# Kernel optimization log

Measured on AMD Instinct MI355X. Metric: run time of the kernel, lower is better.

Reference implementation:

```python
import jax, jax.numpy as jnp
import numpy as np

E, N, NB = 250000, 20000, 8
D_EDGE, D_RBF, D_CBF, D_TRI = 128, 16, 16, 64
INV_SQRT_2 = 1.0 / np.sqrt(2.0).astype(np.float32)
INV_SQRT_NB = 1.0 / np.sqrt(float(NB))


def setup_inputs() -> dict:
    key = jax.random.key(0)
    ks = jax.random.split(key, 13)
    def w(k, fi, fo):
        return (jax.random.normal(k, (fi, fo), dtype=jnp.float32) / np.sqrt(fi)).astype(jnp.float32)
    return {
        "m_st": jax.random.normal(ks[0], (E, D_EDGE), dtype=jnp.float32),
        "rbf": jax.random.normal(ks[1], (E, D_RBF), dtype=jnp.float32),
        "cbf": jax.random.normal(ks[2], (E, NB, D_CBF), dtype=jnp.float32),
        "idx_s": jax.random.randint(ks[3], (E,), 0, N),
        "idx_swap": jax.random.randint(ks[4], (E,), 0, E),
        "basis_idx1": jax.random.randint(ks[5], (N, NB), 0, E),
        "W_m_rbf": w(ks[6], D_EDGE, D_EDGE),
        "W_rbf": w(ks[7], D_RBF, D_EDGE),
        "W_m_cbf": w(ks[8], D_EDGE, D_TRI),
        "W_cbf": w(ks[9], D_CBF, D_TRI),
        "W_dir": w(ks[10], D_TRI, D_EDGE),
        "W_st": w(ks[11], D_EDGE, D_EDGE),
        "W_ts": w(ks[12], D_EDGE, D_EDGE),
    }


def reference(m_st, rbf, cbf, idx_s, idx_swap, basis_idx1,
              W_m_rbf, W_rbf, W_m_cbf, W_cbf, W_dir, W_st, W_ts):
    act = jax.nn.silu
    # gather per-edge basis indices: (E, NB) -> (E*NB,)
    b1 = basis_idx1[idx_s].reshape(-1)
    # rbf branch (ScaleFactor == 1.0 at init -> identity)
    m = act(m_st @ W_m_rbf)                     # (E, D_EDGE)
    m = m * (rbf @ W_rbf)                       # (E, D_EDGE)
    # cbf branch
    e, nb, c = cbf.shape
    cbf2 = cbf.reshape(e * nb, c)               # (E*NB, D_CBF)
    m_nb = act(m @ W_m_cbf)                     # (E, D_TRI)
    m_nb = m_nb[b1]                             # gather -> (E*NB, D_TRI)
    m_nb = m_nb * (cbf2 @ W_cbf)                # (E*NB, D_TRI)
    x = m_nb.reshape(e, nb, -1).sum(1) * INV_SQRT_NB  # (E, D_TRI)
    x = act(x @ W_dir)                          # (E, D_EDGE)
    x_st = act(x @ W_st)
    x_ts = act(x @ W_ts)[idx_swap]              # swap-gather
    return (x_st + x_ts) * INV_SQRT_2
```

## Files before the change

### kernel.cpp

```cpp
#include <hip/hip_runtime.h>


#define DEV __device__ __forceinline__

typedef __attribute__((ext_vector_type(8))) short bf16x8;
typedef __attribute__((ext_vector_type(4))) float f32x4;

constexpr int E = 250000;
constexpr float INV_SQRT_2  = 0.70710678118654752f;
constexpr float INV_SQRT_NB = 0.35355339059327373f;

constexpr int PW1 = 0;
constexpr int PW2 = 16384;
constexpr int PW3 = 20480;
constexpr int PWD = 28672;
constexpr int PWS = 36864;
constexpr int PWT = 53248;
constexpr int PWC = 69632;
constexpr int PACK_TOTAL = 72192;

constexpr size_t OFF_T = 1u << 18;

DEV unsigned short f2bf(float f) {
  unsigned u = __float_as_uint(f);
  return (unsigned short)((u + 0x7fffu + ((u >> 16) & 1u)) >> 16);
}
DEV float bf2f(unsigned short h) { return __uint_as_float((unsigned)h << 16); }
DEV float silu_f(float x) { return x / (1.f + __expf(-x)); }

__global__ __launch_bounds__(256) void k0_pack(
    const float* __restrict__ W1, const float* __restrict__ W2,
    const float* __restrict__ W3, const float* __restrict__ Wc,
    const float* __restrict__ Wd, const float* __restrict__ Ws,
    const float* __restrict__ Wt, unsigned short* __restrict__ pack) {
  int idx = blockIdx.x * 256 + threadIdx.x;
  if (idx >= PACK_TOTAL) return;
  float v = 0.f;
  if (idx < PW2)      { int i = idx;       int n = i >> 7, k = i & 127; v = W1[k * 128 + n]; }
  else if (idx < PW3) { int i = idx - PW2; int n = i >> 5, k = i & 31;  v = (k < 16) ? W2[k * 128 + n] : 0.f; }
  else if (idx < PWD) { int i = idx - PW3; int n = i >> 7, k = i & 127; v = W3[k * 64 + n]; }
  else if (idx < PWS) { int i = idx - PWD; int n = i >> 6, k = i & 63;  v = Wd[k * 128 + n]; }
  else if (idx < PWT) { int i = idx - PWS; int n = i >> 7, k = i & 127; v = Ws[k * 128 + n]; }
  else if (idx < PWC) { int i = idx - PWT; int n = i >> 7, k = i & 127; v = Wt[k * 128 + n]; }
  else                { int i = idx - PWC; int n = i / 40, k = i % 40;  v = (k < 16) ? Wc[k * 64 + n] : 0.f; }
  pack[idx] = f2bf(v);
}

__global__ __launch_bounds__(512) void k1_mbranch(
    const float* __restrict__ m_st, const float* __restrict__ rbf,
    const unsigned short* __restrict__ pack, unsigned short* __restrict__ tT) {
  __shared__ __align__(16) unsigned short sA[128 * 136];
  __shared__ __align__(16) unsigned short sR[128 * 40];
  const int tid = threadIdx.x;
  const int e0 = blockIdx.x * 128;

  #pragma unroll
  for (int it = 0; it < 16; ++it) {
    int i = tid + it * 512;
    int row = i >> 6, kh = i & 63;
    int er = min(e0 + row, E - 1);
    const float2 v = *(const float2*)(m_st + (size_t)er * 128 + kh * 2);
    unsigned pk = (unsigned)f2bf(v.x) | ((unsigned)f2bf(v.y) << 16);
    *(unsigned*)(sA + row * 136 + kh * 2) = pk;
  }
  #pragma unroll
  for (int it = 0; it < 4; ++it) {
    int i = tid + it * 512;
    int row = i >> 4, kh = i & 15;
    int er = min(e0 + row, E - 1);
    unsigned pk = 0;
    if (kh < 8) {
      const float2 v = *(const float2*)(rbf + (size_t)er * 16 + kh * 2);
      pk = (unsigned)f2bf(v.x) | ((unsigned)f2bf(v.y) << 16);
    }
    *(unsigned*)(sR + row * 40 + kh * 2) = pk;
  }
  __syncthreads();

  const int lane = tid & 63, wv = tid >> 6;
  const int m = lane & 15, q = lane >> 4;
  const int arow = wv * 16 + m;

  const f32x4 zero4 = {0.f, 0.f, 0.f, 0.f};
  f32x4 macc[8], racc[8];
  #pragma unroll
  for (int nt = 0; nt < 8; ++nt) { macc[nt] = zero4; racc[nt] = zero4; }

  {
    bf16x8 a = *(const bf16x8*)(sR + arow * 40 + q * 8);
    #pragma unroll
    for (int nt = 0; nt < 8; ++nt) {
      bf16x8 b = *(const bf16x8*)(pack + PW2 + (nt * 16 + m) * 32 + q * 8);
      racc[nt] = __builtin_amdgcn_mfma_f32_16x16x32_bf16(a, b, racc[nt], 0, 0, 0);
    }
  }
  #pragma unroll
  for (int kk = 0; kk < 4; ++kk) {
    bf16x8 a = *(const bf16x8*)(sA + arow * 136 + kk * 32 + q * 8);
    #pragma unroll
    for (int nt = 0; nt < 8; ++nt) {
      bf16x8 b = *(const bf16x8*)(pack + PW1 + (nt * 16 + m) * 128 + kk * 32 + q * 8);
      macc[nt] = __builtin_amdgcn_mfma_f32_16x16x32_bf16(a, b, macc[nt], 0, 0, 0);
    }
  }
  #pragma unroll
  for (int nt = 0; nt < 8; ++nt)
    #pragma unroll
    for (int r = 0; r < 4; ++r) {
      float v = silu_f(macc[nt][r]) * racc[nt][r];
      sA[(wv * 16 + q * 4 + r) * 136 + nt * 16 + m] = f2bf(v);
    }
  __syncthreads();

  f32x4 tacc[4];
  #pragma unroll
  for (int nt = 0; nt < 4; ++nt) tacc[nt] = zero4;
  #pragma unroll
  for (int kk = 0; kk < 4; ++kk) {
    bf16x8 a = *(const bf16x8*)(sA + arow * 136 + kk * 32 + q * 8);
    #pragma unroll
    for (int nt = 0; nt < 4; ++nt) {
      bf16x8 b = *(const bf16x8*)(pack + PW3 + (nt * 16 + m) * 128 + kk * 32 + q * 8);
      tacc[nt] = __builtin_amdgcn_mfma_f32_16x16x32_bf16(a, b, tacc[nt], 0, 0, 0);
    }
  }
  #pragma unroll
  for (int r = 0; r < 4; ++r) {
    int erow = e0 + wv * 16 + q * 4 + r;
    if (erow < E) {
      ushort4 o;
      o.x = f2bf(silu_f(tacc[0][r]));
      o.y = f2bf(silu_f(tacc[1][r]));
      o.z = f2bf(silu_f(tacc[2][r]));
      o.w = f2bf(silu_f(tacc[3][r]));
      *(ushort4*)(tT + (size_t)erow * 64 + m * 4) = o;
    }
  }
}

DEV void xtile_gather_reduce(
    const float* __restrict__ cbf, const int* __restrict__ sB,
    const unsigned short* __restrict__ tT, const bf16x8* bw,
    unsigned short* __restrict__ sX,
    int wv, int m, int q, long long rowA, long long rowB, int mt) {
  bf16x8 af = {0, 0, 0, 0, 0, 0, 0, 0};
  if (q < 2) {
    long long row = (m < 8) ? rowA + m : rowB + (m - 8);
    const float4 c0 = *(const float4*)(cbf + row * 16 + q * 8);
    const float4 c1 = *(const float4*)(cbf + row * 16 + q * 8 + 4);
    af[0] = (short)f2bf(c0.x); af[1] = (short)f2bf(c0.y);
    af[2] = (short)f2bf(c0.z); af[3] = (short)f2bf(c0.w);
    af[4] = (short)f2bf(c1.x); af[5] = (short)f2bf(c1.y);
    af[6] = (short)f2bf(c1.z); af[7] = (short)f2bf(c1.w);
  }
  const f32x4 zero4 = {0.f, 0.f, 0.f, 0.f};
  f32x4 p0 = zero4, p1 = zero4, p2 = zero4, p3 = zero4;
  p0 = __builtin_amdgcn_mfma_f32_16x16x32_bf16(af, bw[0], p0, 0, 0, 0);
  p1 = __builtin_amdgcn_mfma_f32_16x16x32_bf16(af, bw[1], p1, 0, 0, 0);
  p2 = __builtin_amdgcn_mfma_f32_16x16x32_bf16(af, bw[2], p2, 0, 0, 0);
  p3 = __builtin_amdgcn_mfma_f32_16x16x32_bf16(af, bw[3], p3, 0, 0, 0);

  float s0 = 0.f, s1 = 0.f, s2 = 0.f, s3 = 0.f;
  const int lrb = wv * 128 + mt * 16;
  #pragma unroll
  for (int r = 0; r < 4; ++r) {
    int brow = sB[lrb + q * 4 + r];
    ushort4 tv = *(const ushort4*)(tT + (size_t)brow * 64 + m * 4);
    s0 += bf2f(tv.x) * p0[r];
    s1 += bf2f(tv.y) * p1[r];
    s2 += bf2f(tv.z) * p2[r];
    s3 += bf2f(tv.w) * p3[r];
  }
  s0 += __shfl_xor(s0, 16);
  s1 += __shfl_xor(s1, 16);
  s2 += __shfl_xor(s2, 16);
  s3 += __shfl_xor(s3, 16);

  int lrow = wv * 16 + mt * 2 + (q >> 1);
  if (q == 0 || q == 2) {
    sX[lrow * 72 +  0 + m] = f2bf(s0 * INV_SQRT_NB);
    sX[lrow * 72 + 16 + m] = f2bf(s1 * INV_SQRT_NB);
    sX[lrow * 72 + 32 + m] = f2bf(s2 * INV_SQRT_NB);
    sX[lrow * 72 + 48 + m] = f2bf(s3 * INV_SQRT_NB);
  }
}

DEV void ytile(const unsigned short* __restrict__ pack,
               const unsigned short* __restrict__ sX,
               unsigned short* __restrict__ sY, int wv, int m, int q) {
  const int arow = wv * 16 + m;
  const f32x4 zero4 = {0.f, 0.f, 0.f, 0.f};
  f32x4 yacc[8];
  #pragma unroll
  for (int nt = 0; nt < 8; ++nt) yacc[nt] = zero4;
  #pragma unroll
  for (int kk = 0; kk < 2; ++kk) {
    bf16x8 a = *(const bf16x8*)(sX + arow * 72 + kk * 32 + q * 8);
    #pragma unroll
    for (int nt = 0; nt < 8; ++nt) {
      bf16x8 b = *(const bf16x8*)(pack + PWD + (nt * 16 + m) * 64 + kk * 32 + q * 8);
      yacc[nt] = __builtin_amdgcn_mfma_f32_16x16x32_bf16(a, b, yacc[nt], 0, 0, 0);
    }
  }
  #pragma unroll
  for (int nt = 0; nt < 8; ++nt)
    #pragma unroll
    for (int r = 0; r < 4; ++r)
      sY[(wv * 16 + q * 4 + r) * 136 + nt * 16 + m] = f2bf(silu_f(yacc[nt][r]));
}

__global__ __launch_bounds__(512) void k2_fused(
    const float* __restrict__ cbf, const int* __restrict__ idx_s,
    const int* __restrict__ basis_idx1, const unsigned short* __restrict__ pack,
    const unsigned short* __restrict__ tT, float* __restrict__ out) {
  __shared__ __align__(16) unsigned short sWc[64 * 40];
  __shared__ int sB1[1024];
  __shared__ __align__(16) unsigned short sX[128 * 72];
  __shared__ __align__(16) unsigned short sY[128 * 136];
  const int tid = threadIdx.x;
  const int e0 = blockIdx.x * 128;

  ((uint2*)sWc)[tid] = ((const uint2*)(pack + PWC))[tid];
  if (tid < 128) ((uint2*)sWc)[512 + tid] = ((const uint2*)(pack + PWC))[512 + tid];
  #pragma unroll
  for (int it = 0; it < 2; ++it) {
    int i = tid + it * 512;
    int e = min(e0 + (i >> 3), E - 1);
    int b = basis_idx1[idx_s[e] * 8 + (i & 7)];
    sB1[i] = min(max(b, 0), E - 1);
  }
  __syncthreads();

  const int lane = tid & 63, wv = tid >> 6;
  const int m = lane & 15, q = lane >> 4;

  bf16x8 bw[4];
  #pragma unroll
  for (int nt = 0; nt < 4; ++nt)
    bw[nt] = *(const bf16x8*)(sWc + (nt * 16 + m) * 40 + q * 8);

  for (int mt = 0; mt < 8; ++mt) {
    int ea = min(e0 + wv * 16 + mt * 2, E - 1);
    int eb = min(ea + 1, E - 1);
    xtile_gather_reduce(cbf, sB1, tT, bw, sX, wv, m, q,
                        (long long)ea * 8, (long long)eb * 8, mt);
  }
  __syncthreads();

  ytile(pack, sX, sY, wv, m, q);
  __syncthreads();

  const int arow = wv * 16 + m;
  const f32x4 zero4 = {0.f, 0.f, 0.f, 0.f};
  f32x4 acc[8];
  #pragma unroll
  for (int nt = 0; nt < 8; ++nt) acc[nt] = zero4;
  #pragma unroll
  for (int kk = 0; kk < 4; ++kk) {
    bf16x8 a = *(const bf16x8*)(sY + arow * 136 + kk * 32 + q * 8);
    #pragma unroll
    for (int nt = 0; nt < 8; ++nt) {
      bf16x8 b = *(const bf16x8*)(pack + PWS + (nt * 16 + m) * 128 + kk * 32 + q * 8);
      acc[nt] = __builtin_amdgcn_mfma_f32_16x16x32_bf16(a, b, acc[nt], 0, 0, 0);
    }
  }
  #pragma unroll
  for (int nt = 0; nt < 8; ++nt)
    #pragma unroll
    for (int r = 0; r < 4; ++r) {
      int erow = e0 + wv * 16 + q * 4 + r;
      if (erow < E) out[(size_t)erow * 128 + nt * 16 + m] = silu_f(acc[nt][r]);
    }
}

__global__ __launch_bounds__(512) void k3_swap(
    const float* __restrict__ cbf, const int* __restrict__ idx_s,
    const int* __restrict__ idx_swap, const int* __restrict__ basis_idx1,
    const unsigned short* __restrict__ pack, const unsigned short* __restrict__ tT,
    float* __restrict__ out) {
  __shared__ __align__(16) unsigned short sWc[64 * 40];
  __shared__ int sSE[128];
  __shared__ int sB3[1024];
  __shared__ __align__(16) unsigned short sX[128 * 72];
  __shared__ __align__(16) unsigned short sY[128 * 136];
  const int tid = threadIdx.x;
  const int e0 = blockIdx.x * 128;

  ((uint2*)sWc)[tid] = ((const uint2*)(pack + PWC))[tid];
  if (tid < 128) {
    ((uint2*)sWc)[512 + tid] = ((const uint2*)(pack + PWC))[512 + tid];
    int f = idx_swap[min(e0 + tid, E - 1)];
    sSE[tid] = min(max(f, 0), E - 1);
  }
  __syncthreads();
  #pragma unroll
  for (int it = 0; it < 2; ++it) {
    int i = tid + it * 512;
    int f = sSE[i >> 3];
    int b = basis_idx1[idx_s[f] * 8 + (i & 7)];
    sB3[i] = min(max(b, 0), E - 1);
  }
  __syncthreads();

  const int lane = tid & 63, wv = tid >> 6;
  const int m = lane & 15, q = lane >> 4;

  bf16x8 bw[4];
  #pragma unroll
  for (int nt = 0; nt < 4; ++nt)
    bw[nt] = *(const bf16x8*)(sWc + (nt * 16 + m) * 40 + q * 8);

  for (int mt = 0; mt < 8; ++mt) {
    int le = wv * 16 + mt * 2;
    long long fa = sSE[le], fb = sSE[le + 1];
    xtile_gather_reduce(cbf, sB3, tT, bw, sX, wv, m, q, fa * 8, fb * 8, mt);
  }
  __syncthreads();

  ytile(pack, sX, sY, wv, m, q);
  __syncthreads();

  const int arow = wv * 16 + m;
  const f32x4 zero4 = {0.f, 0.f, 0.f, 0.f};
  f32x4 acc[8];
  #pragma unroll
  for (int nt = 0; nt < 8; ++nt) acc[nt] = zero4;
  #pragma unroll
  for (int kk = 0; kk < 4; ++kk) {
    bf16x8 a = *(const bf16x8*)(sY + arow * 136 + kk * 32 + q * 8);
    #pragma unroll
    for (int nt = 0; nt < 8; ++nt) {
      bf16x8 b = *(const bf16x8*)(pack + PWT + (nt * 16 + m) * 128 + kk * 32 + q * 8);
      acc[nt] = __builtin_amdgcn_mfma_f32_16x16x32_bf16(a, b, acc[nt], 0, 0, 0);
    }
  }
  #pragma unroll
  for (int nt = 0; nt < 8; ++nt)
    #pragma unroll
    for (int r = 0; r < 4; ++r) {
      int erow = e0 + wv * 16 + q * 4 + r;
      if (erow < E) {
        size_t o = (size_t)erow * 128 + nt * 16 + m;
        out[o] = (out[o] + silu_f(acc[nt][r])) * INV_SQRT_2;
      }
    }
}

extern "C" void kernel_launch(void* const* d_in, const int* in_sizes, int n_in,
                              void* d_out, int out_size, void* d_ws, size_t ws_size,
                              hipStream_t stream) {
  const float* m_st = (const float*)d_in[0];
  const float* rbf  = (const float*)d_in[1];
  const float* cbf  = (const float*)d_in[2];
  const int* idx_s  = (const int*)d_in[3];
  const int* idx_sw = (const int*)d_in[4];
  const int* bidx   = (const int*)d_in[5];
  const float* W1 = (const float*)d_in[6];
  const float* W2 = (const float*)d_in[7];
  const float* W3 = (const float*)d_in[8];
  const float* Wc = (const float*)d_in[9];
  const float* Wd = (const float*)d_in[10];
  const float* Ws = (const float*)d_in[11];
  const float* Wt = (const float*)d_in[12];

  unsigned short* pack = (unsigned short*)d_ws;
  unsigned short* tT   = (unsigned short*)((char*)d_ws + OFF_T);
  float* out = (float*)d_out;

  const int nb = (E + 127) / 128;
  k0_pack<<<(PACK_TOTAL + 255) / 256, 256, 0, stream>>>(W1, W2, W3, Wc, Wd, Ws, Wt, pack);
  k1_mbranch<<<nb, 512, 0, stream>>>(m_st, rbf, pack, tT);
  k2_fused<<<nb, 512, 0, stream>>>(cbf, idx_s, bidx, pack, tT, out);
  k3_swap<<<nb, 512, 0, stream>>>(cbf, idx_s, idx_sw, bidx, pack, tT, out);
}
```

Measured before the change: 723.2 us.

## Compute the W_ts branch in the fused kernel and gather via a combine pass

k2_fused now also runs the W_ts GEMM on the tile it already holds and writes silu(x@W_ts) for every edge into a workspace buffer. A light k3_combine kernel then gathers that buffer by idx_swap and adds it into the output. Before, k3_swap recomputed the whole cbf/gather/W_dir chain for the swapped edges. This costs an extra fp32 intermediate of E×128 written and randomly read back, and it only takes effect when the workspace is large enough, otherwise the old path runs.

```diff
diff --git a/kernel.cpp b/kernel.cpp
--- a/kernel.cpp
+++ b/kernel.cpp
@@ -20,6 +20,8 @@
 constexpr int PACK_TOTAL = 72192;
 
 constexpr size_t OFF_T = 1u << 18;
+constexpr size_t OFF_Z = OFF_T + (size_t)E * 64 * 2;
+constexpr size_t WS_NEED_FAST = OFF_Z + (size_t)E * 128 * 4;
 
 DEV unsigned short f2bf(float f) {
   unsigned u = __float_as_uint(f);
@@ -212,7 +214,8 @@
 __global__ __launch_bounds__(512) void k2_fused(
     const float* __restrict__ cbf, const int* __restrict__ idx_s,
     const int* __restrict__ basis_idx1, const unsigned short* __restrict__ pack,
-    const unsigned short* __restrict__ tT, float* __restrict__ out) {
+    const unsigned short* __restrict__ tT, float* __restrict__ out,
+    float* __restrict__ zbuf) {
   __shared__ __align__(16) unsigned short sWc[64 * 40];
   __shared__ int sB1[1024];
   __shared__ __align__(16) unsigned short sX[128 * 72];
@@ -271,6 +274,44 @@
       int erow = e0 + wv * 16 + q * 4 + r;
       if (erow < E) out[(size_t)erow * 128 + nt * 16 + m] = silu_f(acc[nt][r]);
     }
+
+  if (zbuf) {
+    #pragma unroll
+    for (int nt = 0; nt < 8; ++nt) acc[nt] = zero4;
+    #pragma unroll
+    for (int kk = 0; kk < 4; ++kk) {
+      bf16x8 a = *(const bf16x8*)(sY + arow * 136 + kk * 32 + q * 8);
+      #pragma unroll
+      for (int nt = 0; nt < 8; ++nt) {
+        bf16x8 b = *(const bf16x8*)(pack + PWT + (nt * 16 + m) * 128 + kk * 32 + q * 8);
+        acc[nt] = __builtin_amdgcn_mfma_f32_16x16x32_bf16(a, b, acc[nt], 0, 0, 0);
+      }
+    }
+    #pragma unroll
+    for (int nt = 0; nt < 8; ++nt)
+      #pragma unroll
+      for (int r = 0; r < 4; ++r) {
+        int erow = e0 + wv * 16 + q * 4 + r;
+        if (erow < E) zbuf[(size_t)erow * 128 + nt * 16 + m] = silu_f(acc[nt][r]);
+      }
+  }
+}
+
+__global__ __launch_bounds__(256) void k3_combine(
+    const int* __restrict__ idx_swap, const float* __restrict__ zbuf,
+    float* __restrict__ out) {
+  int t = blockIdx.x * 256 + threadIdx.x;
+  int e = t >> 5, c = t & 31;
+  if (e >= E) return;
+  int f = idx_swap[e];
+  f = min(max(f, 0), E - 1);
+  float4 o = ((const float4*)out)[t];
+  float4 z = ((const float4*)zbuf)[(size_t)f * 32 + c];
+  o.x = (o.x + z.x) * INV_SQRT_2;
+  o.y = (o.y + z.y) * INV_SQRT_2;
+  o.z = (o.z + z.z) * INV_SQRT_2;
+  o.w = (o.w + z.w) * INV_SQRT_2;
+  ((float4*)out)[t] = o;
 }
 
 __global__ __launch_bounds__(512) void k3_swap(
@@ -365,11 +406,16 @@
 
   unsigned short* pack = (unsigned short*)d_ws;
   unsigned short* tT   = (unsigned short*)((char*)d_ws + OFF_T);
+  float* zbuf = (ws_size >= WS_NEED_FAST) ? (float*)((char*)d_ws + OFF_Z) : nullptr;
   float* out = (float*)d_out;
 
   const int nb = (E + 127) / 128;
   k0_pack<<<(PACK_TOTAL + 255) / 256, 256, 0, stream>>>(W1, W2, W3, Wc, Wd, Ws, Wt, pack);
   k1_mbranch<<<nb, 512, 0, stream>>>(m_st, rbf, pack, tT);
-  k2_fused<<<nb, 512, 0, stream>>>(cbf, idx_s, bidx, pack, tT, out);
-  k3_swap<<<nb, 512, 0, stream>>>(cbf, idx_s, idx_sw, bidx, pack, tT, out);
-}
+  k2_fused<<<nb, 512, 0, stream>>>(cbf, idx_s, bidx, pack, tT, out, zbuf);
+  if (zbuf) {
+    k3_combine<<<(E * 32 + 255) / 256, 256, 0, stream>>>(idx_sw, zbuf, out);
+  } else {
+    k3_swap<<<nb, 512, 0, stream>>>(cbf, idx_s, idx_sw, bidx, pack, tT, out);
+  }
+}
```

Measured after the change: 655.1 us. -9.4%, faster.
